# Optimization experiments

Measured on AMD Instinct MI355X. Metric: run time of the kernel, lower is better.

The kernel has to match this reference:

```python
import jax, jax.numpy as jnp
import numpy as np

B, S, D, H = 4, 2048, 2048, 16
HD = D // H  # 128


def _rope(t, cos, sin):
    # t: [B, S, H, HD]; cos/sin: [S, HD//2]
    tr = t.reshape(t.shape[:-1] + (HD // 2, 2))
    t1, t2 = tr[..., 0], tr[..., 1]
    c = cos[None, :, None, :]
    s = sin[None, :, None, :]
    o1 = t1 * c - t2 * s
    o2 = t1 * s + t2 * c
    return jnp.stack([o1, o2], axis=-1).reshape(t.shape)


def setup_inputs() -> dict:
    key = jax.random.key(0)
    ks = jax.random.split(key, 9)
    init_std = HD ** -0.5
    pos = jnp.arange(S, dtype=jnp.float32)[:, None]
    inv = 1.0 / (10000.0 ** (jnp.arange(0, HD, 2, dtype=jnp.float32) / HD))
    ang = pos * inv[None, :]
    return {
        "x": jax.random.normal(ks[0], (B, S, D), jnp.float32),
        "query": jax.random.normal(ks[1], (B, S, D), jnp.float32),
        "value": jax.random.normal(ks[2], (B, S, D), jnp.float32),
        "freqs_cos": jnp.cos(ang),
        "freqs_sin": jnp.sin(ang),
        "key_w": jax.random.normal(ks[3], (D, D), jnp.float32) * init_std,
        "key_b": jnp.zeros((D,), jnp.float32),
        "proj_w": jax.random.normal(ks[4], (D, D), jnp.float32) * init_std,
        "proj_b": jnp.zeros((D,), jnp.float32),
    }


def reference(x, query, value, freqs_cos, freqs_sin, key_w, key_b, proj_w, proj_b):
    # key projection applied to x; query/value arrive pre-projected
    k = (jnp.einsum("bsd,ed->bse", x, key_w) + key_b).reshape(B, S, H, HD)
    q = query.reshape(B, S, H, HD)
    v = value.reshape(B, S, H, HD)
    q = _rope(q, freqs_cos, freqs_sin)
    k = _rope(k, freqs_cos, freqs_sin)
    scale = 1.0 / np.sqrt(HD)
    scores = jnp.einsum("bqhd,bkhd->bhqk", q, k) * scale  # [B,H,S,S]
    causal = jnp.tril(jnp.ones((S, S), bool))
    scores = jnp.where(causal[None, None], scores, jnp.finfo(scores.dtype).min)
    probs = jax.nn.softmax(scores, axis=-1)
    out = jnp.einsum("bhqk,bkhd->bqhd", probs, v).reshape(B, S, D)
    return jnp.einsum("bsd,ed->bse", out, proj_w) + proj_b
```

## Files before the change

### kernel.cpp

```cpp
#include <hip/hip_runtime.h>
#include <hip/hip_bf16.h>
#include <stdint.h>

#define BB 4
#define SS 2048
#define DD 2048
#define HH 16
#define HD 128
#define MTOT (BB*SS)

typedef __attribute__((ext_vector_type(8))) short short8;
typedef __attribute__((ext_vector_type(4))) float f32x4;

__device__ __forceinline__ unsigned short f2bf(float f) {
    union { float f; unsigned int u; } v; v.f = f;
    unsigned int u = v.u;
    return (unsigned short)((u + 0x7FFFu + ((u >> 16) & 1u)) >> 16);
}
__device__ __forceinline__ unsigned short f2bf_ru(float f) {
    union { float f; unsigned int u; } v; v.f = f;
    return (unsigned short)((v.u + 0x8000u) >> 16);
}

__global__ __launch_bounds__(256) void convert_kernel(
    const float* __restrict__ src, unsigned short* __restrict__ dst, int n4) {
    int i = blockIdx.x * 256 + threadIdx.x;
    if (i >= n4) return;
    float4 v = ((const float4*)src)[i];
    unsigned int lo = (unsigned int)f2bf(v.x) | ((unsigned int)f2bf(v.y) << 16);
    unsigned int hi = (unsigned int)f2bf(v.z) | ((unsigned int)f2bf(v.w) << 16);
    ((uint2*)dst)[i] = make_uint2(lo, hi);
}

__global__ __launch_bounds__(256) void rope_q_kernel(
    const float* __restrict__ q, const float* __restrict__ fc,
    const float* __restrict__ fs, unsigned short* __restrict__ dst) {
    int idx = blockIdx.x * 256 + threadIdx.x;
    int row   = idx >> 10;
    int s     = row & (SS - 1);
    int p     = idx & 63;
    float2 t = ((const float2*)q)[idx];
    float c = fc[s*64 + p], sn = fs[s*64 + p];
    float o1 = t.x*c - t.y*sn;
    float o2 = t.x*sn + t.y*c;
    ((unsigned int*)dst)[idx] = (unsigned int)f2bf(o1) | ((unsigned int)f2bf(o2) << 16);
}

__global__ __launch_bounds__(256) void transpose_v_kernel(
    const float* __restrict__ v, unsigned short* __restrict__ vt) {
    __shared__ unsigned short tile[64][72];
    int bh = blockIdx.z;
    int s0 = blockIdx.x * 64, d0 = blockIdx.y * 64;
    int t = threadIdx.x;
    #pragma unroll
    for (int it = 0; it < 4; ++it) {
        int i  = it*16 + (t >> 4);
        int j4 = t & 15;
        float4 f = *(const float4*)(v +
            (((size_t)((bh >> 4)*SS + s0 + i)*HH + (bh & 15))*HD + d0 + j4*4));
        unsigned int lo = (unsigned int)f2bf(f.x) | ((unsigned int)f2bf(f.y) << 16);
        unsigned int hi = (unsigned int)f2bf(f.z) | ((unsigned int)f2bf(f.w) << 16);
        *(uint2*)&tile[i][j4*4] = make_uint2(lo, hi);
    }
    __syncthreads();
    unsigned int* vt32 = (unsigned int*)vt;
    #pragma unroll
    for (int it = 0; it < 8; ++it) {
        int task = it*256 + t;
        int sp = task & 31;
        int d  = task >> 5;
        unsigned int lo = tile[2*sp][d], hi = tile[2*sp + 1][d];
        vt32[((size_t)bh*HD + d0 + d)*(SS/2) + (s0 >> 1) + sp] = lo | (hi << 16);
    }
}

template<int MODE>
__global__ __launch_bounds__(256, 2) void gemm_kernel(
    const unsigned short* __restrict__ A, const unsigned short* __restrict__ W,
    const float* __restrict__ bias, const float* __restrict__ fc,
    const float* __restrict__ fs, void* __restrict__ out)
{
    __shared__ unsigned short As[128*32];
    __shared__ unsigned short Bs[128*32];
    const int K = DD;
    int L   = blockIdx.y * 16 + blockIdx.x;
    int swz = (L & 7) * 128 + (L >> 3);
    int m0 = (swz >> 4) * 128, n0 = (swz & 15) * 128;
    int t = threadIdx.x, lane = t & 63, w = t >> 6;
    int wm = w >> 1, wn = w & 1;
    int l15 = lane & 15, quad = lane >> 4;

    f32x4 acc[4][4] = {};

    for (int k0 = 0; k0 < K; k0 += 32) {
        __syncthreads();
        #pragma unroll
        for (int i = 0; i < 2; ++i) {
            int ci  = i*256 + t;
            int row = ci >> 2;
            int ce  = (ci & 3) * 8;
            const unsigned short* ga = A + (size_t)(m0 + row) * K + k0 + ce;
            const unsigned short* gb = W + (size_t)(n0 + row) * K + k0 + ce;
            unsigned short* la = As + (size_t)(i*256 + w*64) * 8;
            unsigned short* lb = Bs + (size_t)(i*256 + w*64) * 8;
            __builtin_amdgcn_global_load_lds(
                (__attribute__((address_space(1))) void*)(uintptr_t)ga,
                (__attribute__((address_space(3))) void*)la, 16, 0, 0);
            __builtin_amdgcn_global_load_lds(
                (__attribute__((address_space(1))) void*)(uintptr_t)gb,
                (__attribute__((address_space(3))) void*)lb, 16, 0, 0);
        }
        __syncthreads();

        short8 af[4], bw[4];
        #pragma unroll
        for (int i = 0; i < 4; ++i) {
            af[i] = *(const short8*)(As + (size_t)(wm*64 + i*16 + l15)*32 + quad*8);
            bw[i] = *(const short8*)(Bs + (size_t)(wn*64 + i*16 + l15)*32 + quad*8);
        }
        #pragma unroll
        for (int i = 0; i < 4; ++i)
            #pragma unroll
            for (int j = 0; j < 4; ++j)
                acc[i][j] = __builtin_amdgcn_mfma_f32_16x16x32_bf16(
                    af[i], bw[j], acc[i][j], 0, 0, 0);
    }

    #pragma unroll
    for (int i = 0; i < 4; ++i) {
        #pragma unroll
        for (int j = 0; j < 4; ++j) {
            int col = n0 + wn*64 + j*16 + l15;
            float bv = bias[col];
            #pragma unroll
            for (int r = 0; r < 4; ++r) {
                int row = m0 + wm*64 + i*16 + quad*4 + r;
                float v = acc[i][j][r] + bv;
                if (MODE == 0) {
                    int s = row & (SS - 1);
                    int p = (col & 127) >> 1;
                    float other = __shfl_xor(v, 1);
                    float c = fc[s*64 + p], sn = fs[s*64 + p];
                    float res = (col & 1) ? (other*sn + v*c) : (v*c - other*sn);
                    ((unsigned short*)out)[(size_t)row*DD + col] = f2bf(res);
                } else {
                    ((float*)out)[(size_t)row*DD + col] = v;
                }
            }
        }
    }
}

__global__ __launch_bounds__(512, 4) void attn_kernel(
    const unsigned short* __restrict__ Q, const unsigned short* __restrict__ Kr,
    const unsigned short* __restrict__ Vt, unsigned short* __restrict__ O)
{
    constexpr int PSTR = 72;
    __shared__ unsigned short Ks[64*128];
    __shared__ unsigned short VTs[128*64];
    __shared__ unsigned short Ps[128*PSTR];

    int L   = blockIdx.y * 8 + blockIdx.x;
    int swz = (L & 7) * 64 + (L >> 3);
    int bh   = swz >> 3;
    int pair = swz & 7;

    int b = bh >> 4, h = bh & 15;
    size_t base  = (size_t)b*SS*DD + (size_t)h*HD;
    size_t vbase = (size_t)bh*HD*SS;

    int t = threadIdx.x, lane = t & 63, w = t >> 6;
    int l15 = lane & 15, quad = lane >> 4;
    int l7 = l15 & 7;

    const float scl2 = 0.08838834764831845f * 1.44269504088896f;

    for (int ph = 0; ph < 2; ++ph) {
        int qt = ph ? (15 - pair) : pair;
        int q0 = qt * 128;
        int rw = q0 + w*16;

        short8 aq[4];
        #pragma unroll
        for (int kk = 0; kk < 4; ++kk)
            aq[kk] = *(const short8*)(Q + base +
                (size_t)(rw + l15)*DD + kk*32 + quad*8);

        float m_i[4], l_i[4];
        #pragma unroll
        for (int r = 0; r < 4; ++r) { m_i[r] = -1e30f; l_i[r] = 0.f; }
        f32x4 o_acc[8] = {};

        int jmax = 2*qt + 1;
        for (int jt = 0; jt <= jmax; ++jt) {
            int j0 = jt * 64;

            __syncthreads();
            #pragma unroll
            for (int i = 0; i < 2; ++i) {
                int ci  = i*512 + t;
                int row = ci >> 4;
                int cc  = ci & 15;
                int gch = cc ^ (row & 7);
                const unsigned short* ga =
                    Kr + base + (size_t)(j0 + row)*DD + gch*8;
                unsigned short* la = Ks + (size_t)(i*512 + w*64) * 8;
                __builtin_amdgcn_global_load_lds(
                    (__attribute__((address_space(1))) void*)(uintptr_t)ga,
                    (__attribute__((address_space(3))) void*)la, 16, 0, 0);
            }
            #pragma unroll
            for (int i = 0; i < 2; ++i) {
                int ci  = i*512 + t;
                int d   = ci >> 3;
                int cc  = ci & 7;
                int gch = cc ^ (d & 7);
                const unsigned short* ga =
                    Vt + vbase + (size_t)d*SS + j0 + gch*8;
                unsigned short* la = VTs + (size_t)(i*512 + w*64) * 8;
                __builtin_amdgcn_global_load_lds(
                    (__attribute__((address_space(1))) void*)(uintptr_t)ga,
                    (__attribute__((address_space(3))) void*)la, 16, 0, 0);
            }
            __syncthreads();

            if (j0 > rw + 15) continue;

            f32x4 sacc[4];
            #pragma unroll
            for (int c = 0; c < 4; ++c) {
                sacc[c] = (f32x4){0.f, 0.f, 0.f, 0.f};
                #pragma unroll
                for (int kk = 0; kk < 4; ++kk) {
                    short8 bk = *(const short8*)(Ks +
                        (size_t)(c*16 + l15)*128 + ((kk*4 + quad) ^ l7)*8);
                    sacc[c] = __builtin_amdgcn_mfma_f32_16x16x32_bf16(aq[kk], bk, sacc[c], 0,0,0);
                }
            }

            bool diag = (j0 + 63 > rw);
            float p[4][4], mt4[4];
            #pragma unroll
            for (int r = 0; r < 4; ++r) mt4[r] = -1e30f;
            #pragma unroll
            for (int c = 0; c < 4; ++c)
                #pragma unroll
                for (int r = 0; r < 4; ++r) {
                    float v = sacc[c][r] * scl2;
                    if (diag) {
                        int cg = j0 + c*16 + l15;
                        int rg = rw + quad*4 + r;
                        if (cg > rg) v = -1e30f;
                    }
                    p[c][r] = v;
                    mt4[r] = fmaxf(mt4[r], v);
                }

            bool grow = false;
            #pragma unroll
            for (int r = 0; r < 4; ++r) {
                float m = mt4[r];
                m = fmaxf(m, __shfl_xor(m, 1));
                m = fmaxf(m, __shfl_xor(m, 2));
                m = fmaxf(m, __shfl_xor(m, 4));
                m = fmaxf(m, __shfl_xor(m, 8));
                mt4[r] = m;
                grow = grow || (m > m_i[r] + 8.0f);
            }
            if (__any(grow)) {
                #pragma unroll
                for (int r = 0; r < 4; ++r) {
                    float mn = fmaxf(m_i[r], mt4[r]);
                    float a  = exp2f(m_i[r] - mn);
                    m_i[r] = mn;
                    l_i[r] *= a;
                    mt4[r] = a;
                }
                #pragma unroll
                for (int f = 0; f < 8; ++f)
                    #pragma unroll
                    for (int r = 0; r < 4; ++r)
                        o_acc[f][r] *= mt4[r];
            }

            float rs[4] = {0.f, 0.f, 0.f, 0.f};
            #pragma unroll
            for (int c = 0; c < 4; ++c)
                #pragma unroll
                for (int r = 0; r < 4; ++r) {
                    float e = exp2f(p[c][r] - m_i[r]);
                    rs[r] += e;
                    Ps[(size_t)(w*16 + quad*4 + r)*PSTR + c*16 + l15] = f2bf_ru(e);
                }
            #pragma unroll
            for (int r = 0; r < 4; ++r) {
                float s = rs[r];
                s += __shfl_xor(s, 1);
                s += __shfl_xor(s, 2);
                s += __shfl_xor(s, 4);
                s += __shfl_xor(s, 8);
                l_i[r] += s;
            }

            #pragma unroll
            for (int kk2 = 0; kk2 < 2; ++kk2) {
                short8 ap = *(const short8*)(Ps + (size_t)(w*16 + l15)*PSTR + kk2*32 + quad*8);
                #pragma unroll
                for (int f = 0; f < 8; ++f) {
                    short8 bv = *(const short8*)(VTs +
                        (size_t)(f*16 + l15)*64 + ((kk2*4 + quad) ^ l7)*8);
                    o_acc[f] = __builtin_amdgcn_mfma_f32_16x16x32_bf16(ap, bv, o_acc[f], 0,0,0);
                }
            }
        }

        #pragma unroll
        for (int f = 0; f < 8; ++f) {
            #pragma unroll
            for (int r = 0; r < 4; ++r) {
                int srow = rw + quad*4 + r;
                int d = f*16 + l15;
                O[base + (size_t)srow*DD + d] = f2bf(o_acc[f][r] / l_i[r]);
            }
        }
    }
}

extern "C" void kernel_launch(void* const* d_in, const int* in_sizes, int n_in,
                              void* d_out, int out_size, void* d_ws, size_t ws_size,
                              hipStream_t stream) {
    const float* x      = (const float*)d_in[0];
    const float* query  = (const float*)d_in[1];
    const float* value  = (const float*)d_in[2];
    const float* fc     = (const float*)d_in[3];
    const float* fs     = (const float*)d_in[4];
    const float* key_w  = (const float*)d_in[5];
    const float* key_b  = (const float*)d_in[6];
    const float* proj_w = (const float*)d_in[7];
    const float* proj_b = (const float*)d_in[8];

    const int ND  = BB*SS*DD;
    const int NW  = DD*DD;
    unsigned short* xb  = (unsigned short*)d_ws;
    unsigned short* kwb = xb  + ND;
    unsigned short* pwb = kwb + NW;
    unsigned short* qr  = pwb + NW;
    unsigned short* vt  = qr  + ND;
    unsigned short* kr  = vt  + ND;
    unsigned short* ao  = xb;

    convert_kernel<<<ND/4/256, 256, 0, stream>>>(x, xb, ND/4);
    convert_kernel<<<NW/4/256, 256, 0, stream>>>(key_w, kwb, NW/4);
    convert_kernel<<<NW/4/256, 256, 0, stream>>>(proj_w, pwb, NW/4);
    rope_q_kernel<<<ND/2/256, 256, 0, stream>>>(query, fc, fs, qr);
    transpose_v_kernel<<<dim3(SS/64, HD/64, BB*HH), 256, 0, stream>>>(value, vt);

    dim3 gg(DD/128, MTOT/128);
    gemm_kernel<0><<<gg, 256, 0, stream>>>(xb, kwb, key_b, fc, fs, (void*)kr);
    attn_kernel<<<dim3(8, BB*HH), 512, 0, stream>>>(qr, kr, vt, ao);
    gemm_kernel<1><<<gg, 256, 0, stream>>>(ao, pwb, proj_b, nullptr, nullptr, d_out);
}
```

Before: 577.8 us.

## Double-buffer K/V tiles in attention and vectorize P stores via permuted V layout

The attention loop now keeps two LDS buffers for K and V^T. The next tile's async global-to-LDS loads are issued right after the single per-iteration barrier, so they overlap with the current tile's QK, softmax and PV work, and one of the two barriers per iteration goes away. The probability tile is written as one 8-byte store per row instead of four scalar stores. To allow this, key order inside each 64-key block is permuted, and the V transpose kernel now writes V^T in the matching order. The extra buffers roughly raise LDS use from 50KB to 82KB per block, which likely cuts how many blocks fit on a CU and may cost latency hiding.

```diff
diff --git a/kernel.cpp b/kernel.cpp
--- a/kernel.cpp
+++ b/kernel.cpp
@@ -67,10 +67,11 @@
     #pragma unroll
     for (int it = 0; it < 8; ++it) {
         int task = it*256 + t;
-        int sp = task & 31;
+        int tt = task & 31;
         int d  = task >> 5;
-        unsigned int lo = tile[2*sp][d], hi = tile[2*sp + 1][d];
-        vt32[((size_t)bh*HD + d0 + d)*(SS/2) + (s0 >> 1) + sp] = lo | (hi << 16);
+        int slo = ((tt & 1) << 5) + (tt >> 1);
+        unsigned int lo = tile[slo][d], hi = tile[slo + 16][d];
+        vt32[((size_t)bh*HD + d0 + d)*(SS/2) + (s0 >> 1) + tt] = lo | (hi << 16);
     }
 }
 
@@ -156,8 +157,8 @@
     const unsigned short* __restrict__ Vt, unsigned short* __restrict__ O)
 {
     constexpr int PSTR = 72;
-    __shared__ unsigned short Ks[64*128];
-    __shared__ unsigned short VTs[128*64];
+    __shared__ unsigned short Ks[2*64*128];
+    __shared__ unsigned short VTs[2*128*64];
     __shared__ unsigned short Ps[128*PSTR];
 
     int L   = blockIdx.y * 8 + blockIdx.x;
@@ -175,6 +176,34 @@
 
     const float scl2 = 0.08838834764831845f * 1.44269504088896f;
 
+    auto stage = [&](int jt, int buf) {
+        int j0s = jt * 64;
+        #pragma unroll
+        for (int i = 0; i < 2; ++i) {
+            int ci  = i*512 + t;
+            int row = ci >> 4;
+            int cc  = ci & 15;
+            int gch = cc ^ (row & 7);
+            const unsigned short* ga = Kr + base + (size_t)(j0s + row)*DD + gch*8;
+            unsigned short* la = Ks + buf*(64*128) + (size_t)(i*512 + w*64)*8;
+            __builtin_amdgcn_global_load_lds(
+                (__attribute__((address_space(1))) void*)(uintptr_t)ga,
+                (__attribute__((address_space(3))) void*)la, 16, 0, 0);
+        }
+        #pragma unroll
+        for (int i = 0; i < 2; ++i) {
+            int ci  = i*512 + t;
+            int d   = ci >> 3;
+            int cc  = ci & 7;
+            int gch = cc ^ (d & 7);
+            const unsigned short* ga = Vt + vbase + (size_t)d*SS + j0s + gch*8;
+            unsigned short* la = VTs + buf*(128*64) + (size_t)(i*512 + w*64)*8;
+            __builtin_amdgcn_global_load_lds(
+                (__attribute__((address_space(1))) void*)(uintptr_t)ga,
+                (__attribute__((address_space(3))) void*)la, 16, 0, 0);
+        }
+    };
+
     for (int ph = 0; ph < 2; ++ph) {
         int qt = ph ? (15 - pair) : pair;
         int q0 = qt * 128;
@@ -191,38 +220,18 @@
         for (int r = 0; r < 4; ++r) { m_i[r] = -1e30f; l_i[r] = 0.f; }
         f32x4 o_acc[8] = {};
 
+        __syncthreads();
+        stage(0, 0);
         int jmax = 2*qt + 1;
+
         for (int jt = 0; jt <= jmax; ++jt) {
+            int pb = jt & 1;
             int j0 = jt * 64;
+            const unsigned short* Kb = Ks  + pb*(64*128);
+            const unsigned short* Vb = VTs + pb*(128*64);
 
             __syncthreads();
-            #pragma unroll
-            for (int i = 0; i < 2; ++i) {
-                int ci  = i*512 + t;
-                int row = ci >> 4;
-                int cc  = ci & 15;
-                int gch = cc ^ (row & 7);
-                const unsigned short* ga =
-                    Kr + base + (size_t)(j0 + row)*DD + gch*8;
-                unsigned short* la = Ks + (size_t)(i*512 + w*64) * 8;
-                __builtin_amdgcn_global_load_lds(
-                    (__attribute__((address_space(1))) void*)(uintptr_t)ga,
-                    (__attribute__((address_space(3))) void*)la, 16, 0, 0);
-            }
-            #pragma unroll
-            for (int i = 0; i < 2; ++i) {
-                int ci  = i*512 + t;
-                int d   = ci >> 3;
-                int cc  = ci & 7;
-                int gch = cc ^ (d & 7);
-                const unsigned short* ga =
-                    Vt + vbase + (size_t)d*SS + j0 + gch*8;
-                unsigned short* la = VTs + (size_t)(i*512 + w*64) * 8;
-                __builtin_amdgcn_global_load_lds(
-                    (__attribute__((address_space(1))) void*)(uintptr_t)ga,
-                    (__attribute__((address_space(3))) void*)la, 16, 0, 0);
-            }
-            __syncthreads();
+            if (jt < jmax) stage(jt + 1, pb ^ 1);
 
             if (j0 > rw + 15) continue;
 
@@ -232,14 +241,14 @@
                 sacc[c] = (f32x4){0.f, 0.f, 0.f, 0.f};
                 #pragma unroll
                 for (int kk = 0; kk < 4; ++kk) {
-                    short8 bk = *(const short8*)(Ks +
+                    short8 bk = *(const short8*)(Kb +
                         (size_t)(c*16 + l15)*128 + ((kk*4 + quad) ^ l7)*8);
                     sacc[c] = __builtin_amdgcn_mfma_f32_16x16x32_bf16(aq[kk], bk, sacc[c], 0,0,0);
                 }
             }
 
             bool diag = (j0 + 63 > rw);
-            float p[4][4], mt4[4];
+            float pp[4][4], mt4[4];
             #pragma unroll
             for (int r = 0; r < 4; ++r) mt4[r] = -1e30f;
             #pragma unroll
@@ -252,7 +261,7 @@
                         int rg = rw + quad*4 + r;
                         if (cg > rg) v = -1e30f;
                     }
-                    p[c][r] = v;
+                    pp[c][r] = v;
                     mt4[r] = fmaxf(mt4[r], v);
                 }
 
@@ -283,15 +292,18 @@
                         o_acc[f][r] *= mt4[r];
             }
 
-            float rs[4] = {0.f, 0.f, 0.f, 0.f};
-            #pragma unroll
-            for (int c = 0; c < 4; ++c)
-                #pragma unroll
-                for (int r = 0; r < 4; ++r) {
-                    float e = exp2f(p[c][r] - m_i[r]);
-                    rs[r] += e;
-                    Ps[(size_t)(w*16 + quad*4 + r)*PSTR + c*16 + l15] = f2bf_ru(e);
-                }
+            float rs[4];
+            #pragma unroll
+            for (int r = 0; r < 4; ++r) {
+                float e0 = exp2f(pp[0][r] - m_i[r]);
+                float e1 = exp2f(pp[1][r] - m_i[r]);
+                float e2 = exp2f(pp[2][r] - m_i[r]);
+                float e3 = exp2f(pp[3][r] - m_i[r]);
+                rs[r] = (e0 + e1) + (e2 + e3);
+                unsigned int lo = (unsigned int)f2bf_ru(e0) | ((unsigned int)f2bf_ru(e1) << 16);
+                unsigned int hi = (unsigned int)f2bf_ru(e2) | ((unsigned int)f2bf_ru(e3) << 16);
+                *(uint2*)&Ps[(size_t)(w*16 + quad*4 + r)*PSTR + l15*4] = make_uint2(lo, hi);
+            }
             #pragma unroll
             for (int r = 0; r < 4; ++r) {
                 float s = rs[r];
@@ -307,7 +319,7 @@
                 short8 ap = *(const short8*)(Ps + (size_t)(w*16 + l15)*PSTR + kk2*32 + quad*8);
                 #pragma unroll
                 for (int f = 0; f < 8; ++f) {
-                    short8 bv = *(const short8*)(VTs +
+                    short8 bv = *(const short8*)(Vb +
                         (size_t)(f*16 + l15)*64 + ((kk2*4 + quad) ^ l7)*8);
                     o_acc[f] = __builtin_amdgcn_mfma_f32_16x16x32_bf16(ap, bv, o_acc[f], 0,0,0);
                 }
```

New measurement: 592.0 us. +2.5%, slower.
